# Optimization experiments

Measured on AMD Instinct MI355X. Metric: run time of the kernel, lower is better.

The kernel has to match this reference:

```python
import jax, jax.numpy as jnp
from jax import lax
import numpy as np

DIM = 256
D_STATE = 16
D_CONV = 4
EXPAND = 2
D_INNER = EXPAND * DIM          # 512
DT_RANK = (DIM + 15) // 16      # 16
EPS = 1e-5


def setup_inputs() -> dict:
    key = jax.random.key(0)
    ks = jax.random.split(key, 8)
    B, H, W = 8, 32, 32
    dt_init = 0.01  # softplus(b_dt) ~= dt_init at init (mamba-style)
    return {
        "x": jax.random.normal(ks[0], (B, DIM, H, W), jnp.float32),
        "ln_gamma": jnp.ones((DIM,), jnp.float32),
        "ln_beta": jnp.zeros((DIM,), jnp.float32),
        "W_in": jax.random.normal(ks[1], (DIM, 2 * D_INNER), jnp.float32) * 0.02,
        "conv_w": jax.random.normal(ks[2], (D_INNER, D_CONV), jnp.float32) * 0.2,
        "conv_b": jnp.zeros((D_INNER,), jnp.float32),
        "W_xproj": jax.random.normal(ks[3], (D_INNER, DT_RANK + 2 * D_STATE), jnp.float32) * 0.02,
        "W_dt": jax.random.normal(ks[4], (DT_RANK, D_INNER), jnp.float32) * 0.05,
        "b_dt": jnp.full((D_INNER,), float(np.log(np.expm1(dt_init))), jnp.float32),
        "A_log": jnp.log(jnp.broadcast_to(
            jnp.arange(1, D_STATE + 1, dtype=jnp.float32), (D_INNER, D_STATE))),
        "D_skip": jnp.ones((D_INNER,), jnp.float32),
        "W_out": jax.random.normal(ks[5], (D_INNER, DIM), jnp.float32) * 0.02,
    }


def _mamba_layer(x, ln_gamma, ln_beta, W_in, conv_w, conv_b, W_xproj,
                 W_dt, b_dt, A_log, D_skip, W_out):
    B, C, H, W = x.shape
    L = H * W
    # (B,C,H,W) -> (B, L, C)
    xf = x.transpose(0, 2, 3, 1).reshape(B, L, C)
    # LayerNorm over channel dim
    mu = xf.mean(-1, keepdims=True)
    var = ((xf - mu) ** 2).mean(-1, keepdims=True)
    xn = (xf - mu) * lax.rsqrt(var + EPS) * ln_gamma + ln_beta
    # in_proj -> u (ssm branch) and z (gate branch)
    xz = xn @ W_in                              # [B, L, 2*D_INNER]
    u, z = xz[..., :D_INNER], xz[..., D_INNER:]
    # causal depthwise conv1d over L, then SiLU
    uc = u.transpose(0, 2, 1)                   # [B, D_INNER, L]
    uc = lax.conv_general_dilated(
        uc, conv_w[:, None, :], window_strides=(1,),
        padding=[(D_CONV - 1, 0)], feature_group_count=D_INNER)
    u2 = jax.nn.silu(uc + conv_b[None, :, None]).transpose(0, 2, 1)  # [B, L, D_INNER]
    # input-dependent dt, B, C
    dbc = u2 @ W_xproj                          # [B, L, DT_RANK + 2*D_STATE]
    dt = jax.nn.softplus(dbc[..., :DT_RANK] @ W_dt + b_dt)            # [B, L, D_INNER]
    Bm = dbc[..., DT_RANK:DT_RANK + D_STATE]    # [B, L, D_STATE]
    Cm = dbc[..., DT_RANK + D_STATE:]           # [B, L, D_STATE]
    A = -jnp.exp(A_log)                         # [D_INNER, D_STATE]

    def step(h, ins):
        dt_t, B_t, C_t, u_t = ins               # [B,Din], [B,S], [B,S], [B,Din]
        dA = jnp.exp(dt_t[:, :, None] * A)      # [B, Din, S]
        h = dA * h + dt_t[:, :, None] * B_t[:, None, :] * u_t[:, :, None]
        y = jnp.einsum('bds,bs->bd', h, C_t)
        return h, y

    h0 = jnp.zeros((B, D_INNER, D_STATE), xf.dtype)
    xs = (dt.transpose(1, 0, 2), Bm.transpose(1, 0, 2),
          Cm.transpose(1, 0, 2), u2.transpose(1, 0, 2))
    _, ys = lax.scan(step, h0, xs)              # ys: [L, B, D_INNER]
    y = ys.transpose(1, 0, 2) + u2 * D_skip     # skip connection D*u
    y = y * jax.nn.silu(z)                      # gate
    o = y @ W_out                               # [B, L, C]
    return o.reshape(B, H, W, C).transpose(0, 3, 1, 2) + x


def reference(x, ln_gamma, ln_beta, W_in, conv_w, conv_b, W_xproj,
              W_dt, b_dt, A_log, D_skip, W_out):
    return _mamba_layer(x, ln_gamma, ln_beta, W_in, conv_w, conv_b, W_xproj,
                        W_dt, b_dt, A_log, D_skip, W_out)
```

## Files before the change

### kernel.cpp

```cpp
#include <hip/hip_runtime.h>
#include <hip/hip_bf16.h>
#include <math.h>

#define DIMC   256
#define DI     512
#define DS     16
#define DTR    16
#define NX     48
#define BATCH  8
#define LSEQ   1024
#define MROWS  8192
#define CHUNK  64
#define NC     (LSEQ / CHUNK)

typedef __attribute__((ext_vector_type(8))) short short8;
typedef __attribute__((ext_vector_type(4))) float f32x4;

__device__ __forceinline__ unsigned short f2bf(float v) {
  __hip_bfloat16 h = __float2bfloat16(v);
  return *reinterpret_cast<unsigned short*>(&h);
}
__device__ __forceinline__ float bf2f(unsigned short u) {
  return __int_as_float(((int)u) << 16);
}

__device__ __forceinline__ float dpp_sum16(float v) {
  float t;
  t = __int_as_float(__builtin_amdgcn_mov_dpp(__float_as_int(v), 0xB1,  0xF, 0xF, true)); v += t;
  t = __int_as_float(__builtin_amdgcn_mov_dpp(__float_as_int(v), 0x4E,  0xF, 0xF, true)); v += t;
  t = __int_as_float(__builtin_amdgcn_mov_dpp(__float_as_int(v), 0x141, 0xF, 0xF, true)); v += t;
  t = __int_as_float(__builtin_amdgcn_mov_dpp(__float_as_int(v), 0x140, 0xF, 0xF, true)); v += t;
  return v;
}

__global__ __launch_bounds__(256) void prologue(const float* __restrict__ W_in,
                                                const float* __restrict__ W_out,
                                                const float* __restrict__ W_xproj,
                                                const float* __restrict__ W_dt,
                                                const float* __restrict__ x,
                                                const float* __restrict__ gamma,
                                                const float* __restrict__ beta,
                                                unsigned short* __restrict__ Wib,
                                                unsigned short* __restrict__ Wob,
                                                unsigned short* __restrict__ Wxpb,
                                                unsigned short* __restrict__ Wdtb,
                                                unsigned short* __restrict__ xnb) {
  __shared__ float sx[DIMC][67];
  __shared__ float smean[64], srs[64];
  const int blk = blockIdx.x, tid = threadIdx.x;
  if (blk < 384) {
    float (*t)[67] = sx;
    const float* W; unsigned short* Wt; int K, N, bx, by;
    if (blk < 256) { W = W_in;  Wt = Wib; K = DIMC; N = 1024; bx = blk & 31; by = blk >> 5; }
    else           { W = W_out; Wt = Wob; K = DI;   N = DIMC; bx = (blk - 256) & 7; by = (blk - 256) >> 3; }
    int n0 = bx * 32, k0 = by * 32;
    int tx = tid & 31, ty = tid >> 5;
    for (int i = ty; i < 32; i += 8) t[i][tx] = W[(size_t)(k0 + i) * N + n0 + tx];
    __syncthreads();
    for (int i = ty; i < 32; i += 8)
      Wt[(size_t)(n0 + i) * K + k0 + tx] = f2bf(t[tx][i]);
    return;
  }
  if (blk < 512) {
    int idx = (blk - 384) * 256 + tid;
    int n = idx >> 9, k = idx & 511;
    Wxpb[idx] = (n < NX) ? f2bf(W_xproj[(size_t)k * NX + n]) : (unsigned short)0;
    return;
  }
  if (blk < 576) {
    int idx = (blk - 512) * 256 + tid;
    int n = idx >> 5, k = idx & 31;
    Wdtb[idx] = (k < DTR) ? f2bf(W_dt[(size_t)k * DI + n]) : (unsigned short)0;
    return;
  }
  const int lb = blk - 576;
  const int b = lb >> 4, l0 = (lb & 15) * 64;
  {
    const int cbase = tid >> 2;
    const int lp = (tid & 3) * 16;
#pragma unroll
    for (int cg = 0; cg < 4; ++cg) {
      const int c = cg * 64 + cbase;
      const float* p = x + ((size_t)b * DIMC + c) * LSEQ + l0 + lp;
#pragma unroll
      for (int q = 0; q < 4; ++q) {
        float4 v = *(const float4*)(p + q * 4);
        sx[c][lp + q * 4 + 0] = v.x;
        sx[c][lp + q * 4 + 1] = v.y;
        sx[c][lp + q * 4 + 2] = v.z;
        sx[c][lp + q * 4 + 3] = v.w;
      }
    }
  }
  __syncthreads();
  {
    const int lane = tid & 63, w = tid >> 6;
    const int l = (w << 4) + (lane & 15);
    const int quad = lane >> 4;
    float sum = 0.f, sq = 0.f;
#pragma unroll 8
    for (int cc = 0; cc < 64; ++cc) {
      float v = sx[quad * 64 + cc][l];
      sum += v; sq += v * v;
    }
    sum += __shfl_xor(sum, 16); sq += __shfl_xor(sq, 16);
    sum += __shfl_xor(sum, 32); sq += __shfl_xor(sq, 32);
    if (quad == 0) {
      float mean = sum * (1.f / 256.f);
      float var  = sq * (1.f / 256.f) - mean * mean;
      smean[l] = mean; srs[l] = rsqrtf(var + 1e-5f);
    }
  }
  __syncthreads();
  {
    const float gg = gamma[tid], bb = beta[tid];
    const size_t base = ((size_t)b * LSEQ + l0) * DIMC + tid;
#pragma unroll 4
    for (int ll = 0; ll < 64; ++ll) {
      float v = (sx[tid][ll] - smean[ll]) * srs[ll] * gg + bb;
      xnb[base + (size_t)ll * DIMC] = f2bf(v);
    }
  }
}

#define GTM 128
#define GTN 64
#define GBK 32
__global__ __launch_bounds__(256) void gemm_bf16(const unsigned short* __restrict__ A,
                                                 const unsigned short* __restrict__ Bt,
                                                 void* __restrict__ Cout,
                                                 int M, int N, int K, int mode,
                                                 const float* __restrict__ X) {
  __shared__ unsigned short As[GTM][GBK];
  __shared__ unsigned short Bs[GTN][GBK];
  const int tid = threadIdx.x;
  const int lane = tid & 63, wave = tid >> 6;
  const int wm = wave >> 1, wn = wave & 1;
  const int quad = lane >> 4, l16 = lane & 15;
  const int m0 = blockIdx.y * GTM, n0 = blockIdx.x * GTN;

  f32x4 acc[4][2];
#pragma unroll
  for (int i = 0; i < 4; ++i)
#pragma unroll
    for (int j = 0; j < 2; ++j) acc[i][j] = (f32x4){0.f, 0.f, 0.f, 0.f};

  for (int k0 = 0; k0 < K; k0 += GBK) {
#pragma unroll
    for (int q = 0; q < 2; ++q) {
      int id = q * 256 + tid;
      int row = id >> 2, c = id & 3;
      uint4 v = *(const uint4*)(A + (size_t)(m0 + row) * K + k0 + c * 8);
      *(uint4*)&As[row][c * 8] = v;
    }
    {
      int row = tid >> 2, c = tid & 3;
      uint4 v = *(const uint4*)(Bt + (size_t)(n0 + row) * K + k0 + c * 8);
      *(uint4*)&Bs[row][c * 8] = v;
    }
    __syncthreads();
    short8 af[4], bfrag[2];
#pragma unroll
    for (int i = 0; i < 4; ++i)
      af[i] = *(const short8*)&As[wm * 64 + i * 16 + l16][quad * 8];
#pragma unroll
    for (int j = 0; j < 2; ++j)
      bfrag[j] = *(const short8*)&Bs[wn * 32 + j * 16 + l16][quad * 8];
#pragma unroll
    for (int i = 0; i < 4; ++i)
#pragma unroll
      for (int j = 0; j < 2; ++j)
        acc[i][j] = __builtin_amdgcn_mfma_f32_16x16x32_bf16(af[i], bfrag[j], acc[i][j], 0, 0, 0);
    __syncthreads();
  }

  if (mode == 2) {
    unsigned short* Cb = (unsigned short*)Cout;
#pragma unroll
    for (int i = 0; i < 4; ++i) {
      int rowb = wm * 64 + i * 16 + quad * 4;
#pragma unroll
      for (int j = 0; j < 2; ++j) {
        int n = n0 + wn * 32 + j * 16 + l16;
#pragma unroll
        for (int r = 0; r < 4; ++r)
          Cb[(size_t)(m0 + rowb + r) * N + n] = f2bf(acc[i][j][r]);
      }
    }
  } else {
    float* C = (float*)Cout;
#pragma unroll
    for (int i = 0; i < 4; ++i) {
      int m = m0 + wm * 64 + i * 16 + quad * 4;
      int b = m >> 10, l = m & 1023;
#pragma unroll
      for (int j = 0; j < 2; ++j) {
        int n = n0 + wn * 32 + j * 16 + l16;
        size_t o = (size_t)b * (DIMC * LSEQ) + (size_t)n * LSEQ + l;
        f32x4 xv = *(const f32x4*)(X + o);
        f32x4 rv = acc[i][j] + xv;
        *(f32x4*)(C + o) = rv;
      }
    }
  }
}

__global__ __launch_bounds__(256) void conv_silu(const unsigned short* __restrict__ xzb,
                                                 const float* __restrict__ conv_w,
                                                 const float* __restrict__ conv_b,
                                                 unsigned int* __restrict__ u2b) {
  int idx = (blockIdx.x * 256 + threadIdx.x) * 2;
  int c = idx & (DI - 1);
  int m = idx >> 9;
  int l = m & 1023;
  float2 acc = *(const float2*)(conv_b + c);
  float4 w0 = *(const float4*)(conv_w + c * 4);
  float4 w1 = *(const float4*)(conv_w + c * 4 + 4);
  const float wa[4] = {w0.x, w0.y, w0.z, w0.w};
  const float wb[4] = {w1.x, w1.y, w1.z, w1.w};
#pragma unroll
  for (int k = 0; k < 4; ++k) {
    int lj = l - 3 + k;
    if (lj >= 0) {
      unsigned int v = *(const unsigned int*)(xzb + (size_t)(m - 3 + k) * 1024 + c);
      acc.x = fmaf(bf2f((unsigned short)(v & 0xffff)), wa[k], acc.x);
      acc.y = fmaf(bf2f((unsigned short)(v >> 16)),   wb[k], acc.y);
    }
  }
  float vx = acc.x / (1.f + __expf(-acc.x));
  float vy = acc.y / (1.f + __expf(-acc.y));
  u2b[idx >> 1] = (unsigned int)f2bf(vx) | ((unsigned int)f2bf(vy) << 16);
}

__global__ __launch_bounds__(256) void xproj_dt(const unsigned short* __restrict__ u2b,
                                                const unsigned short* __restrict__ Wxpb,
                                                const unsigned short* __restrict__ Wdtb,
                                                const float* __restrict__ b_dt,
                                                float* __restrict__ dbc64,
                                                float* __restrict__ dtv) {
  __shared__ unsigned short Bs[64][512 + 8];
  __shared__ unsigned short sdbc[32][40];
  const int m0 = blockIdx.x * 32;
  const int tid = threadIdx.x, lane = tid & 63, w = tid >> 6;
  const int quad = lane >> 4, l16 = lane & 15;
#pragma unroll
  for (int q = 0; q < 16; ++q) {
    int id = q * 256 + tid;
    int row = id >> 6, c8 = id & 63;
    *(uint4*)&Bs[row][c8 * 8] = *(const uint4*)(Wxpb + (size_t)row * 512 + c8 * 8);
  }
  __syncthreads();
  f32x4 acc[2];
  acc[0] = (f32x4){0.f, 0.f, 0.f, 0.f};
  acc[1] = (f32x4){0.f, 0.f, 0.f, 0.f};
#pragma unroll 4
  for (int k0 = 0; k0 < 512; k0 += 32) {
    short8 af0 = *(const short8*)(u2b + (size_t)(m0 + l16) * 512 + k0 + quad * 8);
    short8 af1 = *(const short8*)(u2b + (size_t)(m0 + 16 + l16) * 512 + k0 + quad * 8);
    short8 bf  = *(const short8*)&Bs[w * 16 + l16][k0 + quad * 8];
    acc[0] = __builtin_amdgcn_mfma_f32_16x16x32_bf16(af0, bf, acc[0], 0, 0, 0);
    acc[1] = __builtin_amdgcn_mfma_f32_16x16x32_bf16(af1, bf, acc[1], 0, 0, 0);
  }
#pragma unroll
  for (int i = 0; i < 2; ++i)
#pragma unroll
    for (int r = 0; r < 4; ++r)
      dbc64[(size_t)(m0 + i * 16 + quad * 4 + r) * 64 + w * 16 + l16] = acc[i][r];
  if (w < 2) {
#pragma unroll
    for (int i = 0; i < 2; ++i)
#pragma unroll
      for (int r = 0; r < 4; ++r)
        sdbc[i * 16 + quad * 4 + r][w * 16 + l16] = f2bf(acc[i][r]);
  }
  __syncthreads();
  short8 af0 = *(const short8*)&sdbc[l16][quad * 8];
  short8 af1 = *(const short8*)&sdbc[16 + l16][quad * 8];
#pragma unroll
  for (int jn = 0; jn < 8; ++jn) {
    const int n0 = w * 128 + jn * 16;
    short8 bf = *(const short8*)(Wdtb + (size_t)(n0 + l16) * 32 + quad * 8);
    f32x4 a0 = (f32x4){0.f, 0.f, 0.f, 0.f}, a1 = a0;
    a0 = __builtin_amdgcn_mfma_f32_16x16x32_bf16(af0, bf, a0, 0, 0, 0);
    a1 = __builtin_amdgcn_mfma_f32_16x16x32_bf16(af1, bf, a1, 0, 0, 0);
    const float bd = b_dt[n0 + l16];
#pragma unroll
    for (int r = 0; r < 4; ++r) {
      float v = a0[r] + bd;
      dtv[(size_t)(m0 + quad * 4 + r) * DI + n0 + l16] = (v > 20.f) ? v : log1pf(__expf(v));
      float v2 = a1[r] + bd;
      dtv[(size_t)(m0 + 16 + quad * 4 + r) * DI + n0 + l16] = (v2 > 20.f) ? v2 : log1pf(__expf(v2));
    }
  }
}

__global__ __launch_bounds__(256) void scan_pass1(const float* __restrict__ dtv,
                                                  const unsigned short* __restrict__ u2b,
                                                  const float* __restrict__ dbc64,
                                                  const float* __restrict__ A_log,
                                                  float* __restrict__ hend,
                                                  float* __restrict__ Ssum) {
  const int bb = blockIdx.x, dblk = blockIdx.y, cc = blockIdx.z;
  const int tid = threadIdx.x;
  const int di = tid >> 4, s = tid & 15;
  const int d = dblk * 16 + di;
  const float Ads = -__expf(A_log[d * DS + s]);

  __shared__ float2 sdu[CHUNK][16];
  __shared__ float  sB[CHUNK][16];
  {
    const int t0 = cc * CHUNK;
#pragma unroll
    for (int q = 0; q < 4; ++q) {
      int lin = q * 256 + tid;
      int tt = lin >> 4, dd = lin & 15;
      size_t m = (size_t)bb * LSEQ + t0 + tt;
      sdu[tt][dd] = make_float2(dtv[m * DI + dblk * 16 + dd],
                                bf2f(u2b[m * DI + dblk * 16 + dd]));
      sB[tt][dd]  = dbc64[m * 64 + DTR + dd];
    }
  }
  __syncthreads();
  float h = 0.f, dtsum = 0.f;
#pragma unroll 4
  for (int tt = 0; tt < CHUNK; ++tt) {
    float2 du = sdu[tt][di];
    float Bv  = sB[tt][s];
    h = fmaf(__expf(du.x * Ads), h, du.x * du.y * Bv);
    dtsum += du.x;
  }
  size_t ci = ((size_t)(bb * NC + cc) * DI + d);
  hend[ci * DS + s] = h;
  if (s == 0) Ssum[ci] = dtsum;
}

__global__ __launch_bounds__(256) void scan_pass2(const float* __restrict__ A_log,
                                                  const float* __restrict__ hend,
                                                  const float* __restrict__ Ssum,
                                                  float* __restrict__ hin) {
  const int bb = blockIdx.x, dblk = blockIdx.y;
  const int tid = threadIdx.x;
  const int di = tid >> 4, s = tid & 15;
  const int d = dblk * 16 + di;
  const float Ads = -__expf(A_log[d * DS + s]);
  float h = 0.f;
  for (int cc = 0; cc < NC; ++cc) {
    size_t ci = ((size_t)(bb * NC + cc) * DI + d);
    hin[ci * DS + s] = h;
    h = fmaf(__expf(Ads * Ssum[ci]), h, hend[ci * DS + s]);
  }
}

__global__ __launch_bounds__(256) void scan_pass3(const float* __restrict__ dtv,
                                                  const unsigned short* __restrict__ u2b,
                                                  const float* __restrict__ dbc64,
                                                  const unsigned short* __restrict__ xzb,
                                                  const float* __restrict__ A_log,
                                                  const float* __restrict__ D_skip,
                                                  const float* __restrict__ hin,
                                                  unsigned short* __restrict__ yb) {
  const int bb = blockIdx.x, dblk = blockIdx.y, cc = blockIdx.z;
  const int tid = threadIdx.x;
  const int di = tid >> 4, s = tid & 15;
  const int d = dblk * 16 + di;
  const float Ads = -__expf(A_log[d * DS + s]);

  __shared__ float2 sdu[CHUNK][16];
  __shared__ float2 sBC[CHUNK][16];
  __shared__ float  sz[CHUNK][16], sy[CHUNK][16];
  const int t0 = cc * CHUNK;
#pragma unroll
  for (int q = 0; q < 4; ++q) {
    int lin = q * 256 + tid;
    int tt = lin >> 4, dd = lin & 15;
    size_t m = (size_t)bb * LSEQ + t0 + tt;
    sdu[tt][dd] = make_float2(dtv[m * DI + dblk * 16 + dd],
                              bf2f(u2b[m * DI + dblk * 16 + dd]));
    sBC[tt][dd] = make_float2(dbc64[m * 64 + DTR + dd], dbc64[m * 64 + DTR + DS + dd]);
    sz [tt][dd] = bf2f(xzb[m * 1024 + DI + dblk * 16 + dd]);
  }
  __syncthreads();
  float h = hin[((size_t)(bb * NC + cc) * DI + d) * DS + s];
#pragma unroll 4
  for (int tt = 0; tt < CHUNK; ++tt) {
    float2 du = sdu[tt][di];
    float2 bc = sBC[tt][s];
    h = fmaf(__expf(du.x * Ads), h, du.x * du.y * bc.x);
    float v = dpp_sum16(h * bc.y);
    if (s == 0) sy[tt][di] = v;
  }
  __syncthreads();
#pragma unroll
  for (int q = 0; q < 4; ++q) {
    int lin = q * 256 + tid;
    int tt = lin >> 4, dd = lin & 15;
    size_t m = (size_t)bb * LSEQ + t0 + tt;
    float yv = sy[tt][dd] + sdu[tt][dd].y * D_skip[dblk * 16 + dd];
    float z = sz[tt][dd];
    yv *= z / (1.f + __expf(-z));
    yb[m * DI + dblk * 16 + dd] = f2bf(yv);
  }
}

extern "C" void kernel_launch(void* const* d_in, const int* in_sizes, int n_in,
                              void* d_out, int out_size, void* d_ws, size_t ws_size,
                              hipStream_t stream) {
  const float* x       = (const float*)d_in[0];
  const float* ln_g    = (const float*)d_in[1];
  const float* ln_b    = (const float*)d_in[2];
  const float* W_in    = (const float*)d_in[3];
  const float* conv_w  = (const float*)d_in[4];
  const float* conv_b  = (const float*)d_in[5];
  const float* W_xproj = (const float*)d_in[6];
  const float* W_dt    = (const float*)d_in[7];
  const float* b_dt    = (const float*)d_in[8];
  const float* A_log   = (const float*)d_in[9];
  const float* D_skip  = (const float*)d_in[10];
  const float* W_out   = (const float*)d_in[11];
  float* out = (float*)d_out;

  float* ws    = (float*)d_ws;
  float* dbc64 = ws;
  float* dtv   = dbc64 + (size_t)MROWS * 64;
  float* hend  = dtv  + (size_t)MROWS * DI;
  float* hin   = hend + (size_t)BATCH * NC * DI * DS;
  float* Ssum  = hin  + (size_t)BATCH * NC * DI * DS;
  unsigned short* xzb  = (unsigned short*)(Ssum + (size_t)BATCH * NC * DI);
  unsigned short* u2b  = xzb + (size_t)MROWS * 1024;
  unsigned short* yb   = u2b + (size_t)MROWS * DI;
  unsigned short* xnb  = yb;
  unsigned short* Wib  = yb  + (size_t)MROWS * DI;
  unsigned short* Wob  = Wib + (size_t)DIMC * 1024;
  unsigned short* Wxpb = Wob + (size_t)DI * DIMC;
  unsigned short* Wdtb = Wxpb + (size_t)64 * 512;

  prologue<<<704, 256, 0, stream>>>(W_in, W_out, W_xproj, W_dt, x, ln_g, ln_b,
                                    Wib, Wob, Wxpb, Wdtb, xnb);

  gemm_bf16<<<dim3(1024 / GTN, MROWS / GTM), 256, 0, stream>>>(
      xnb, Wib, xzb, MROWS, 1024, DIMC, 2, nullptr);

  conv_silu<<<(MROWS * DI) / 512, 256, 0, stream>>>(xzb, conv_w, conv_b,
                                                    (unsigned int*)u2b);

  xproj_dt<<<MROWS / 32, 256, 0, stream>>>(u2b, Wxpb, Wdtb, b_dt, dbc64, dtv);

  dim3 gp13(BATCH, DI / 16, NC);
  dim3 gp2(BATCH, DI / 16);
  scan_pass1<<<gp13, 256, 0, stream>>>(dtv, u2b, dbc64, A_log, hend, Ssum);
  scan_pass2<<<gp2, 256, 0, stream>>>(A_log, hend, Ssum, hin);
  scan_pass3<<<gp13, 256, 0, stream>>>(dtv, u2b, dbc64, xzb, A_log, D_skip, hin, yb);

  gemm_bf16<<<dim3(DIMC / GTN, MROWS / GTM), 256, 0, stream>>>(
      yb, Wob, out, MROWS, DIMC, DI, 1, x);
}
```

Baseline: 205.5 us.

## Pack dt and u as bf16 pairs and fold chunk-carry pass into pass1

```diff
diff --git a/kernel.cpp b/kernel.cpp
--- a/kernel.cpp
+++ b/kernel.cpp
@@ -44,7 +44,8 @@
                                                 unsigned short* __restrict__ Wob,
                                                 unsigned short* __restrict__ Wxpb,
                                                 unsigned short* __restrict__ Wdtb,
-                                                unsigned short* __restrict__ xnb) {
+                                                unsigned short* __restrict__ xnb,
+                                                int* __restrict__ cnt) {
   __shared__ float sx[DIMC][67];
   __shared__ float smean[64], srs[64];
   const int blk = blockIdx.x, tid = threadIdx.x;
@@ -73,6 +74,10 @@
     Wdtb[idx] = (k < DTR) ? f2bf(W_dt[(size_t)k * DI + n]) : (unsigned short)0;
     return;
   }
+  if (blk == 704) {
+    cnt[tid] = 0;
+    return;
+  }
   const int lb = blk - 576;
   const int b = lb >> 4, l0 = (lb & 15) * 64;
   {
@@ -237,7 +242,7 @@
                                                 const unsigned short* __restrict__ Wdtb,
                                                 const float* __restrict__ b_dt,
                                                 float* __restrict__ dbc64,
-                                                float* __restrict__ dtv) {
+                                                unsigned int* __restrict__ dtu) {
   __shared__ unsigned short Bs[64][512 + 8];
   __shared__ unsigned short sdbc[32][40];
   const int m0 = blockIdx.x * 32;
@@ -286,20 +291,27 @@
     const float bd = b_dt[n0 + l16];
 #pragma unroll
     for (int r = 0; r < 4; ++r) {
+      int row0 = m0 + quad * 4 + r;
+      int row1 = row0 + 16;
       float v = a0[r] + bd;
-      dtv[(size_t)(m0 + quad * 4 + r) * DI + n0 + l16] = (v > 20.f) ? v : log1pf(__expf(v));
+      float sp = (v > 20.f) ? v : log1pf(__expf(v));
+      unsigned int u0 = (unsigned int)u2b[(size_t)row0 * DI + n0 + l16];
+      dtu[(size_t)row0 * DI + n0 + l16] = u0 | ((unsigned int)f2bf(sp) << 16);
       float v2 = a1[r] + bd;
-      dtv[(size_t)(m0 + 16 + quad * 4 + r) * DI + n0 + l16] = (v2 > 20.f) ? v2 : log1pf(__expf(v2));
-    }
-  }
-}
-
-__global__ __launch_bounds__(256) void scan_pass1(const float* __restrict__ dtv,
-                                                  const unsigned short* __restrict__ u2b,
+      float sp2 = (v2 > 20.f) ? v2 : log1pf(__expf(v2));
+      unsigned int u1 = (unsigned int)u2b[(size_t)row1 * DI + n0 + l16];
+      dtu[(size_t)row1 * DI + n0 + l16] = u1 | ((unsigned int)f2bf(sp2) << 16);
+    }
+  }
+}
+
+__global__ __launch_bounds__(256) void scan_pass1(const unsigned int* __restrict__ dtu,
                                                   const float* __restrict__ dbc64,
                                                   const float* __restrict__ A_log,
                                                   float* __restrict__ hend,
-                                                  float* __restrict__ Ssum) {
+                                                  float* __restrict__ Ssum,
+                                                  float* __restrict__ hin,
+                                                  int* __restrict__ cnt) {
   const int bb = blockIdx.x, dblk = blockIdx.y, cc = blockIdx.z;
   const int tid = threadIdx.x;
   const int di = tid >> 4, s = tid & 15;
@@ -308,16 +320,23 @@
 
   __shared__ float2 sdu[CHUNK][16];
   __shared__ float  sB[CHUNK][16];
+  __shared__ int slast;
   {
     const int t0 = cc * CHUNK;
 #pragma unroll
-    for (int q = 0; q < 4; ++q) {
-      int lin = q * 256 + tid;
+    for (int q = 0; q < 2; ++q) {
+      int lin = q * 512 + tid * 2;
       int tt = lin >> 4, dd = lin & 15;
       size_t m = (size_t)bb * LSEQ + t0 + tt;
-      sdu[tt][dd] = make_float2(dtv[m * DI + dblk * 16 + dd],
-                                bf2f(u2b[m * DI + dblk * 16 + dd]));
-      sB[tt][dd]  = dbc64[m * 64 + DTR + dd];
+      uint2 du2 = *(const uint2*)(dtu + m * DI + dblk * 16 + dd);
+      f32x4 dv;
+      dv[0] = bf2f((unsigned short)(du2.x >> 16));
+      dv[1] = bf2f((unsigned short)(du2.x & 0xffff));
+      dv[2] = bf2f((unsigned short)(du2.y >> 16));
+      dv[3] = bf2f((unsigned short)(du2.y & 0xffff));
+      *(f32x4*)&sdu[tt][dd] = dv;
+      float2 Bv = *(const float2*)(dbc64 + m * 64 + DTR + dd);
+      *(float2*)&sB[tt][dd] = Bv;
     }
   }
   __syncthreads();
@@ -332,27 +351,23 @@
   size_t ci = ((size_t)(bb * NC + cc) * DI + d);
   hend[ci * DS + s] = h;
   if (s == 0) Ssum[ci] = dtsum;
-}
-
-__global__ __launch_bounds__(256) void scan_pass2(const float* __restrict__ A_log,
-                                                  const float* __restrict__ hend,
-                                                  const float* __restrict__ Ssum,
-                                                  float* __restrict__ hin) {
-  const int bb = blockIdx.x, dblk = blockIdx.y;
-  const int tid = threadIdx.x;
-  const int di = tid >> 4, s = tid & 15;
-  const int d = dblk * 16 + di;
-  const float Ads = -__expf(A_log[d * DS + s]);
-  float h = 0.f;
-  for (int cc = 0; cc < NC; ++cc) {
-    size_t ci = ((size_t)(bb * NC + cc) * DI + d);
-    hin[ci * DS + s] = h;
-    h = fmaf(__expf(Ads * Ssum[ci]), h, hend[ci * DS + s]);
-  }
-}
-
-__global__ __launch_bounds__(256) void scan_pass3(const float* __restrict__ dtv,
-                                                  const unsigned short* __restrict__ u2b,
+
+  __threadfence();
+  if (tid == 0) slast = atomicAdd(&cnt[bb * 32 + dblk], 1);
+  __syncthreads();
+  if (slast == NC - 1) {
+    __threadfence();
+    float hh = 0.f;
+#pragma unroll
+    for (int c2 = 0; c2 < NC; ++c2) {
+      size_t cj = ((size_t)(bb * NC + c2) * DI + d);
+      hin[cj * DS + s] = hh;
+      hh = fmaf(__expf(Ads * Ssum[cj]), hh, hend[cj * DS + s]);
+    }
+  }
+}
+
+__global__ __launch_bounds__(256) void scan_pass3(const unsigned int* __restrict__ dtu,
                                                   const float* __restrict__ dbc64,
                                                   const unsigned short* __restrict__ xzb,
                                                   const float* __restrict__ A_log,
@@ -370,14 +385,26 @@
   __shared__ float  sz[CHUNK][16], sy[CHUNK][16];
   const int t0 = cc * CHUNK;
 #pragma unroll
-  for (int q = 0; q < 4; ++q) {
-    int lin = q * 256 + tid;
+  for (int q = 0; q < 2; ++q) {
+    int lin = q * 512 + tid * 2;
     int tt = lin >> 4, dd = lin & 15;
     size_t m = (size_t)bb * LSEQ + t0 + tt;
-    sdu[tt][dd] = make_float2(dtv[m * DI + dblk * 16 + dd],
-                              bf2f(u2b[m * DI + dblk * 16 + dd]));
-    sBC[tt][dd] = make_float2(dbc64[m * 64 + DTR + dd], dbc64[m * 64 + DTR + DS + dd]);
-    sz [tt][dd] = bf2f(xzb[m * 1024 + DI + dblk * 16 + dd]);
+    uint2 du2 = *(const uint2*)(dtu + m * DI + dblk * 16 + dd);
+    f32x4 dv;
+    dv[0] = bf2f((unsigned short)(du2.x >> 16));
+    dv[1] = bf2f((unsigned short)(du2.x & 0xffff));
+    dv[2] = bf2f((unsigned short)(du2.y >> 16));
+    dv[3] = bf2f((unsigned short)(du2.y & 0xffff));
+    *(f32x4*)&sdu[tt][dd] = dv;
+    float2 Bv = *(const float2*)(dbc64 + m * 64 + DTR + dd);
+    float2 Cv = *(const float2*)(dbc64 + m * 64 + DTR + DS + dd);
+    f32x4 bc;
+    bc[0] = Bv.x; bc[1] = Cv.x; bc[2] = Bv.y; bc[3] = Cv.y;
+    *(f32x4*)&sBC[tt][dd] = bc;
+    unsigned int zz = *(const unsigned int*)(xzb + m * 1024 + DI + dblk * 16 + dd);
+    float2 zv = make_float2(bf2f((unsigned short)(zz & 0xffff)),
+                            bf2f((unsigned short)(zz >> 16)));
+    *(float2*)&sz[tt][dd] = zv;
   }
   __syncthreads();
   float h = hin[((size_t)(bb * NC + cc) * DI + d) * DS + s];
@@ -421,11 +448,12 @@
 
   float* ws    = (float*)d_ws;
   float* dbc64 = ws;
-  float* dtv   = dbc64 + (size_t)MROWS * 64;
-  float* hend  = dtv  + (size_t)MROWS * DI;
+  float* hend  = dbc64 + (size_t)MROWS * 64;
   float* hin   = hend + (size_t)BATCH * NC * DI * DS;
   float* Ssum  = hin  + (size_t)BATCH * NC * DI * DS;
-  unsigned short* xzb  = (unsigned short*)(Ssum + (size_t)BATCH * NC * DI);
+  int*   cnt   = (int*)(Ssum + (size_t)BATCH * NC * DI);
+  unsigned int* dtu = (unsigned int*)(cnt + 256);
+  unsigned short* xzb  = (unsigned short*)(dtu + (size_t)MROWS * DI);
   unsigned short* u2b  = xzb + (size_t)MROWS * 1024;
   unsigned short* yb   = u2b + (size_t)MROWS * DI;
   unsigned short* xnb  = yb;
@@ -434,8 +462,8 @@
   unsigned short* Wxpb = Wob + (size_t)DI * DIMC;
   unsigned short* Wdtb = Wxpb + (size_t)64 * 512;
 
-  prologue<<<704, 256, 0, stream>>>(W_in, W_out, W_xproj, W_dt, x, ln_g, ln_b,
-                                    Wib, Wob, Wxpb, Wdtb, xnb);
+  prologue<<<705, 256, 0, stream>>>(W_in, W_out, W_xproj, W_dt, x, ln_g, ln_b,
+                                    Wib, Wob, Wxpb, Wdtb, xnb, cnt);
 
   gemm_bf16<<<dim3(1024 / GTN, MROWS / GTM), 256, 0, stream>>>(
       xnb, Wib, xzb, MROWS, 1024, DIMC, 2, nullptr);
@@ -443,13 +471,11 @@
   conv_silu<<<(MROWS * DI) / 512, 256, 0, stream>>>(xzb, conv_w, conv_b,
                                                     (unsigned int*)u2b);
 
-  xproj_dt<<<MROWS / 32, 256, 0, stream>>>(u2b, Wxpb, Wdtb, b_dt, dbc64, dtv);
+  xproj_dt<<<MROWS / 32, 256, 0, stream>>>(u2b, Wxpb, Wdtb, b_dt, dbc64, dtu);
 
   dim3 gp13(BATCH, DI / 16, NC);
-  dim3 gp2(BATCH, DI / 16);
-  scan_pass1<<<gp13, 256, 0, stream>>>(dtv, u2b, dbc64, A_log, hend, Ssum);
-  scan_pass2<<<gp2, 256, 0, stream>>>(A_log, hend, Ssum, hin);
-  scan_pass3<<<gp13, 256, 0, stream>>>(dtv, u2b, dbc64, xzb, A_log, D_skip, hin, yb);
+  scan_pass1<<<gp13, 256, 0, stream>>>(dtu, dbc64, A_log, hend, Ssum, hin, cnt);
+  scan_pass3<<<gp13, 256, 0, stream>>>(dtu, dbc64, xzb, A_log, D_skip, hin, yb);
 
   gemm_bf16<<<dim3(DIMC / GTN, MROWS / GTM), 256, 0, stream>>>(
       yb, Wob, out, MROWS, DIMC, DI, 1, x);
```

Result: slower. 506.3 us (+146.4%).
